# Optimization experiments

Measured on AMD Instinct MI355X. Metric: run time of the kernel, lower is better.

The kernel has to match this reference:

```python
import jax, jax.numpy as jnp
import numpy as np

N, DIM, DK, DV = 8192, 512, 128, 512


def setup_inputs() -> dict:
    key = jax.random.key(0)
    ks = jax.random.split(key, 6)
    return {
        "x": jax.random.normal(ks[0], (N, DIM), dtype=jnp.float32),
        "w_w": jax.random.normal(ks[1], (DK, DIM), dtype=jnp.float32) * (1.0 / np.sqrt(DIM)),
        "w_b": jax.random.normal(ks[2], (DK,), dtype=jnp.float32) * 0.01,
        "wv_w": jax.random.normal(ks[3], (DV, DIM), dtype=jnp.float32) * (1.0 / np.sqrt(DIM)),
        "wv_b": jax.random.normal(ks[4], (DV,), dtype=jnp.float32) * 0.01,
        "a": jax.random.normal(ks[5], (2 * DK,), dtype=jnp.float32),
    }


def reference(x, w_w, w_b, wv_w, wv_b, a):
    dk = w_b.shape[0]
    # eqx.nn.Linear: y = W @ x + b, applied per-row via vmap -> x @ W.T + b
    wx = x @ w_w.T + w_b                       # [n, dk]
    e_src = wx @ a[:dk]                        # [n], sum(wx_i * a1)
    e_dst = wx @ a[dk:]                        # [n], sum(wx_j * a2)
    logits = jax.nn.leaky_relu(e_src[:, None] + e_dst[None, :])  # [n, n]
    score = jax.nn.softmax(logits, axis=-1)    # row-wise softmax
    v = x @ wv_w.T + wv_b                      # [n, dv]
    return score @ v                           # [n, dv]
```

## Files before the change

kernel.cpp:

```cpp
#include <hip/hip_runtime.h>
#include <hip/hip_bf16.h>

#define N_   8192
#define DIM_ 512
#define DK_  128
#define DV_  512
#define L2E_ 1.44269504088896f
#define NCH_ 512
#define CHR_ 16

typedef short short8 __attribute__((ext_vector_type(8)));
typedef float f32x4  __attribute__((ext_vector_type(4)));
typedef float f32x2  __attribute__((ext_vector_type(2)));

__device__ __forceinline__ float fexp2(float x) { return __builtin_amdgcn_exp2f(x); }

__device__ __forceinline__ ushort f2bf(float f) {
    union { float f; unsigned u; } v; v.f = f;
    unsigned u = v.u;
    return (ushort)((u + 0x7FFFu + ((u >> 16) & 1u)) >> 16);
}
__device__ __forceinline__ float bf2f(ushort u) { return __uint_as_float(((unsigned)u) << 16); }
__device__ __forceinline__ float decode_max(unsigned u) {
    return __uint_as_float((u & 0x80000000u) ? (u ^ 0x80000000u) : ~u);
}

__global__ __launch_bounds__(256) void prep_kernel(const float* __restrict__ w_w,
                            const float* __restrict__ w_b, const float* __restrict__ a,
                            const float* __restrict__ wv_w,
                            float* __restrict__ u1, float* __restrict__ u2,
                            float* __restrict__ scal, ushort* __restrict__ wvbf) {
    int bid = blockIdx.x, t = threadIdx.x;
    if (bid < 2) {
        int d = bid * 256 + t;
        float s1 = 0.f, s2 = 0.f;
        for (int k = 0; k < DK_; ++k) {
            float w = w_w[k * DIM_ + d];
            s1 += w * a[k];
            s2 += w * a[DK_ + k];
        }
        u1[d] = s1; u2[d] = s2;
        if (d == 0) { float c = 0.f; for (int k = 0; k < DK_; ++k) c += w_b[k] * a[k];        scal[0] = c; }
        if (d == 1) { float c = 0.f; for (int k = 0; k < DK_; ++k) c += w_b[k] * a[DK_ + k];  scal[1] = c; }
        if (d == 2) ((unsigned*)scal)[3] = 0u;
    } else {
        int idx = (bid - 2) * 2048 + t * 8;
        f32x4 lo = *(const f32x4*)(wv_w + idx);
        f32x4 hi = *(const f32x4*)(wv_w + idx + 4);
        short8 f;
#pragma unroll
        for (int e = 0; e < 4; ++e) { f[e] = (short)f2bf(lo[e]); f[e + 4] = (short)f2bf(hi[e]); }
        *(short8*)(wvbf + idx) = f;
    }
}

__global__ __launch_bounds__(256) void e_kernel(const float* __restrict__ x,
        const float* __restrict__ u1, const float* __restrict__ u2,
        const float* __restrict__ scal, float* __restrict__ e_src, float* __restrict__ e_dst,
        ushort* __restrict__ xbf, int* __restrict__ rank, int* __restrict__ ki,
        int* __restrict__ res) {
    int wid = threadIdx.x >> 6, lane = threadIdx.x & 63;
    int row = blockIdx.x * 4 + wid;
    const float* xr = x + (size_t)row * DIM_;
    int d0 = lane * 8;
    f32x4 xa = *(const f32x4*)(xr + d0);
    f32x4 xb = *(const f32x4*)(xr + d0 + 4);
    f32x4 ua = *(const f32x4*)(u1 + d0);
    f32x4 ub = *(const f32x4*)(u1 + d0 + 4);
    f32x4 va = *(const f32x4*)(u2 + d0);
    f32x4 vb = *(const f32x4*)(u2 + d0 + 4);
    short8 xv;
#pragma unroll
    for (int e = 0; e < 4; ++e) { xv[e] = (short)f2bf(xa[e]); xv[e + 4] = (short)f2bf(xb[e]); }
    *(short8*)(xbf + (size_t)row * DIM_ + d0) = xv;
    float s1 = 0.f, s2 = 0.f;
#pragma unroll
    for (int e = 0; e < 4; ++e) {
        s1 += xa[e] * ua[e] + xb[e] * ub[e];
        s2 += xa[e] * va[e] + xb[e] * vb[e];
    }
    for (int off = 32; off; off >>= 1) { s1 += __shfl_xor(s1, off); s2 += __shfl_xor(s2, off); }
    if (lane == 0) {
        e_src[row] = s1 + scal[0];
        e_dst[row] = s2 + scal[1];
    }
    if (lane == 1) rank[row] = 0;
    if (lane == 2) ki[row] = 0;
    if (lane == 3) res[row] = 0;
}

__global__ __launch_bounds__(256) void rankv_kernel(const float* __restrict__ e_dst,
        const float* __restrict__ e_src, int* __restrict__ rank, int* __restrict__ ki,
        int* __restrict__ res, float* __restrict__ scal,
        const ushort* __restrict__ xbf, const ushort* __restrict__ wvbf,
        const float* __restrict__ wv_b, ushort* __restrict__ V) {
    int bid = blockIdx.x, t = threadIdx.x;
    if (bid < 512) {
        __shared__ float ed[512];
        __shared__ float esl[512];
        __shared__ float red[4];
        int bx = bid & 31, by = bid >> 5;
        int rbase = by * 512;
        for (int q = t; q < 512; q += 256) { ed[q] = e_dst[rbase + q]; esl[q] = e_src[rbase + q]; }
        __syncthreads();
        if (bx == 0) {
            float m = fmaxf(ed[t], ed[t + 256]);
            for (int off = 32; off; off >>= 1) m = fmaxf(m, __shfl_xor(m, off));
            if ((t & 63) == 0) red[t >> 6] = m;
            __syncthreads();
            if (t == 0) {
                m = fmaxf(fmaxf(red[0], red[1]), fmaxf(red[2], red[3]));
                unsigned u = __float_as_uint(m);
                u ^= (unsigned)(((int)u >> 31)) | 0x80000000u;
                atomicMax(((unsigned*)scal) + 3, u);
            }
        }
        int j = bx * 256 + t;
        float kj = e_dst[j];
        float kei = -e_src[j];
        float kes = e_src[j];
        int cj = 0, ci = 0, ce = 0;
#pragma unroll 8
        for (int q = 0; q < 512; ++q) {
            float v = ed[q];
            float w = esl[q];
            int r = rbase + q;
            cj += (v < kj) || (v == kj && r < j);
            ci += (v < kei);
            ce += (w < kes) || (w == kes && r < j);
        }
        atomicAdd(rank + j, cj);
        atomicAdd(ki + j, ci);
        atomicAdd(res + j, ce);
    } else {
        int vb = bid - 512;
        int wid = t >> 6, lane = t & 63;
        int ln16 = lane & 15, kg = lane >> 4;
        int jb = (vb & 31) * 256 + wid * 64;
        int cb = (vb >> 5) * 64;
        f32x4 acc[4][4] = {};
        float bias[4];
#pragma unroll
        for (int ng = 0; ng < 4; ++ng) bias[ng] = wv_b[cb + ng * 16 + ln16];
        for (int k0 = 0; k0 < DIM_; k0 += 32) {
            int kk = k0 + kg * 8;
            short8 afr[4], bfr[4];
#pragma unroll
            for (int mg = 0; mg < 4; ++mg)
                afr[mg] = *(const short8*)(xbf + (size_t)(jb + mg * 16 + ln16) * DIM_ + kk);
#pragma unroll
            for (int ng = 0; ng < 4; ++ng)
                bfr[ng] = *(const short8*)(wvbf + (size_t)(cb + ng * 16 + ln16) * DIM_ + kk);
#pragma unroll
            for (int mg = 0; mg < 4; ++mg)
#pragma unroll
                for (int ng = 0; ng < 4; ++ng)
                    acc[mg][ng] = __builtin_amdgcn_mfma_f32_16x16x32_bf16(afr[mg], bfr[ng], acc[mg][ng], 0, 0, 0);
        }
#pragma unroll
        for (int mg = 0; mg < 4; ++mg)
#pragma unroll
            for (int ng = 0; ng < 4; ++ng)
#pragma unroll
                for (int r = 0; r < 4; ++r) {
                    int j = jb + mg * 16 + kg * 4 + r;
                    int c = cb + ng * 16 + ln16;
                    V[(size_t)j * DV_ + c] = f2bf(acc[mg][ng][r] + bias[ng]);
                }
    }
}

__global__ __launch_bounds__(256) void scatter_kernel(const float* __restrict__ e_dst,
        const int* __restrict__ rank, const int* __restrict__ res, const float* __restrict__ scal,
        int* __restrict__ perm, int* __restrict__ perm_es,
        float* __restrict__ Gs1, float* __restrict__ Gs2) {
    int j = blockIdx.x * 256 + threadIdx.x;
    float M = decode_max(((const unsigned*)scal)[3]);
    int rk = rank[j];
    float d = (e_dst[j] - M) * L2E_;
    perm[rk] = j;
    perm_es[res[j]] = j;
    Gs1[rk] = fexp2(d);
    Gs2[rk] = fexp2(0.01f * d);
}

__global__ __launch_bounds__(256) void p1_kernel(const ushort* __restrict__ V,
        const int* __restrict__ perm, const float* __restrict__ Gs1, const float* __restrict__ Gs2,
        unsigned* __restrict__ Pk, float* __restrict__ C1, float* __restrict__ C2,
        float* __restrict__ C1z, float* __restrict__ C2z,
        float* __restrict__ zl2, float* __restrict__ zl1) {
    int ch = blockIdx.x >> 1, half = blockIdx.x & 1;
    int t = threadIdx.x;
    int c = half * 256 + t;
    int k0 = ch * CHR_;
    int   jj[CHR_];
    float g1[CHR_], g2[CHR_], v[CHR_];
#pragma unroll
    for (int r = 0; r < CHR_; ++r) { jj[r] = perm[k0 + r]; g1[r] = Gs1[k0 + r]; g2[r] = Gs2[k0 + r]; }
#pragma unroll
    for (int r = 0; r < CHR_; ++r) v[r] = bf2f(V[(size_t)jj[r] * DV_ + c]);
    float t1 = 0.f, t2 = 0.f;
#pragma unroll
    for (int r = 0; r < CHR_; ++r) { t1 += g1[r] * v[r]; t2 += g2[r] * v[r]; }
    float r2 = 0.f, p1r = 0.f;
#pragma unroll
    for (int r = 0; r < CHR_; ++r) {
        Pk[(size_t)(k0 + r) * DV_ + c] = (unsigned)f2bf(r2) | ((unsigned)f2bf(t1 - p1r) << 16);
        r2 += g2[r] * v[r]; p1r += g1[r] * v[r];
    }
    C1[ch * 512 + c] = t1; C2[ch * 512 + c] = t2;
    if (half == 0 && t == 0) {
        float z1t = 0.f, z2t = 0.f;
#pragma unroll
        for (int r = 0; r < CHR_; ++r) { z1t += g1[r]; z2t += g2[r]; }
        C1z[ch] = z1t; C2z[ch] = z2t;
        float zp2 = 0.f, zp1 = 0.f;
#pragma unroll
        for (int r = 0; r < CHR_; ++r) {
            zl2[k0 + r] = zp2; zl1[k0 + r] = z1t - zp1;
            zp2 += g2[r]; zp1 += g1[r];
        }
    }
    if (ch == NCH_ - 1) {
        Pk[(size_t)N_ * DV_ + c] = 0u;
        if (half == 0 && t == 0) { zl2[N_] = 0.f; zl1[N_] = 0.f; }
    }
}

__global__ __launch_bounds__(256) void p2_kernel(const float* __restrict__ C1,
        const float* __restrict__ C2, const float* __restrict__ C1z, const float* __restrict__ C2z,
        float* __restrict__ pc2, float* __restrict__ scs,
        float* __restrict__ zc2, float* __restrict__ zc1) {
    int b = blockIdx.x, t = threadIdx.x;
    if (b < 64) {
        int colL = t >> 5, s = t & 31;
        int c = b * 8 + colL;
        int base = s * 16;
        float v[16]; float seg = 0.f;
#pragma unroll
        for (int q = 0; q < 16; ++q) { v[q] = C2[(base + q) * 512 + c]; seg += v[q]; }
        float x = seg;
#pragma unroll
        for (int d = 1; d < 32; d <<= 1) { float y = __shfl_up(x, d, 32); if (s >= d) x += y; }
        float run = x - seg;
#pragma unroll
        for (int q = 0; q < 16; ++q) { pc2[(base + q) * 512 + c] = run; run += v[q]; }
        if (s == 31) pc2[NCH_ * 512 + c] = run;
    } else if (b < 128) {
        int colL = t >> 5, s = t & 31;
        int c = (b - 64) * 8 + colL;
        int base = s * 16;
        float v[16]; float seg = 0.f;
#pragma unroll
        for (int q = 0; q < 16; ++q) { v[q] = C1[(base + q) * 512 + c]; seg += v[q]; }
        float x = seg;
#pragma unroll
        for (int d = 1; d < 32; d <<= 1) { float y = __shfl_down(x, d, 32); if (s + d < 32) x += y; }
        float fwd = 0.f;
#pragma unroll
        for (int q = 0; q < 16; ++q) { fwd += v[q]; scs[(base + q) * 512 + c] = x - fwd; }
        if (s == 31) scs[NCH_ * 512 + c] = 0.f;
    } else {
        __shared__ float wt[4];
        bool pre = (b == 128);
        float v0 = pre ? C2z[t * 2] : C1z[t * 2];
        float v1 = pre ? C2z[t * 2 + 1] : C1z[t * 2 + 1];
        float seg = v0 + v1;
        int lane = t & 63, w = t >> 6;
        float x = seg;
        if (pre) {
#pragma unroll
            for (int d = 1; d < 64; d <<= 1) { float y = __shfl_up(x, d); if (lane >= d) x += y; }
            if (lane == 63) wt[w] = x;
        } else {
#pragma unroll
            for (int d = 1; d < 64; d <<= 1) { float y = __shfl_down(x, d); if (lane + d < 64) x += y; }
            if (lane == 0) wt[w] = x;
        }
        __syncthreads();
        float off = 0.f;
        if (pre) {
            for (int u = 0; u < w; ++u) off += wt[u];
            float run = off + (x - seg);
            zc2[t * 2] = run; run += v0; zc2[t * 2 + 1] = run;
            if (t == 255) zc2[NCH_] = off + x;
        } else {
            for (int u = w + 1; u < 4; ++u) off += wt[u];
            float S = off + x;
            zc1[t * 2]     = S - v0;
            zc1[t * 2 + 1] = S - v0 - v1;
            if (t == 255) zc1[NCH_] = 0.f;
        }
    }
}

__global__ __launch_bounds__(256) void out_kernel(const float* __restrict__ e_src,
        const float* __restrict__ scal, const int* __restrict__ ki,
        const int* __restrict__ perm_es,
        const float* __restrict__ zl2, const float* __restrict__ zl1,
        const float* __restrict__ zc2, const float* __restrict__ zc1,
        const float* __restrict__ pc2, const float* __restrict__ scs,
        const unsigned* __restrict__ Pk, float* __restrict__ out) {
    int t = threadIdx.x;
    float M = decode_max(((const unsigned*)scal)[3]);
    int idx0 = blockIdx.x * 16;
    int c2 = t * 2;
#pragma unroll 2
    for (int q = 0; q < 16; ++q) {
        int i = perm_es[idx0 + q];
        float es = e_src[i];
        float tt = es + M;
        float m = fmaxf(tt, 0.01f * tt);
        float F1 = fexp2((tt - m) * L2E_);
        float F2 = fexp2((0.01f * tt - m) * L2E_);
        int lo = ki[i];
        int ch = lo >> 4;
        float z = F2 * (zc2[ch] + zl2[lo]) + F1 * (zc1[ch] + zl1[lo]);
        float rz = 1.0f / z;
        const unsigned* pt = Pk + (size_t)lo * DV_;
        unsigned w0 = pt[c2], w1 = pt[c2 + 1];
        f32x2 cp = *(const f32x2*)(pc2 + ch * 512 + c2);
        f32x2 cs = *(const f32x2*)(scs + ch * 512 + c2);
        float o0 = (F2 * (cp[0] + bf2f((ushort)(w0 & 0xFFFFu))) + F1 * (cs[0] + bf2f((ushort)(w0 >> 16)))) * rz;
        float o1 = (F2 * (cp[1] + bf2f((ushort)(w1 & 0xFFFFu))) + F1 * (cs[1] + bf2f((ushort)(w1 >> 16)))) * rz;
        out[(size_t)i * DV_ + c2]     = o0;
        out[(size_t)i * DV_ + c2 + 1] = o1;
    }
}

extern "C" void kernel_launch(void* const* d_in, const int* in_sizes, int n_in,
                              void* d_out, int out_size, void* d_ws, size_t ws_size,
                              hipStream_t stream) {
    const float* x    = (const float*)d_in[0];
    const float* w_w  = (const float*)d_in[1];
    const float* w_b  = (const float*)d_in[2];
    const float* wv_w = (const float*)d_in[3];
    const float* wv_b = (const float*)d_in[4];
    const float* a    = (const float*)d_in[5];
    float* out = (float*)d_out;
    char* ws = (char*)d_ws;

    ushort*   V    = (ushort*)(ws);
    ushort*   xbf  = (ushort*)(ws + 8388608);
    unsigned* Pk   = (unsigned*)(ws + 16777216);
    char*     sm   = ws + 35651584;
    float*  u1      = (float*)(sm);
    float*  u2      = (float*)(sm + 2048);
    float*  e_src   = (float*)(sm + 4096);
    float*  e_dst   = (float*)(sm + 36864);
    float*  scal    = (float*)(sm + 69632);
    float*  Gs1     = (float*)(sm + 69888);
    float*  Gs2     = (float*)(sm + 102656);
    float*  C1      = (float*)(sm + 135424);
    float*  C2      = (float*)(sm + 1184000);
    float*  pc2     = (float*)(sm + 2232576);
    float*  scs     = (float*)(sm + 3284224);
    float*  C1z     = (float*)(sm + 4335872);
    float*  C2z     = (float*)(sm + 4337920);
    float*  zl2     = (float*)(sm + 4339968);
    float*  zl1     = (float*)(sm + 4372992);
    float*  zc2     = (float*)(sm + 4406016);
    float*  zc1     = (float*)(sm + 4410112);
    int*    perm    = (int*)  (sm + 4414208);
    int*    rank    = (int*)  (sm + 4446976);
    int*    ki      = (int*)  (sm + 4479744);
    int*    res     = (int*)  (sm + 4512512);
    int*    perm_es = (int*)  (sm + 4545280);
    ushort* wvbf    = (ushort*)(sm + 4578048);

    hipLaunchKernelGGL(prep_kernel,    dim3(130),     dim3(256), 0, stream, w_w, w_b, a, wv_w, u1, u2, scal, wvbf);
    hipLaunchKernelGGL(e_kernel,       dim3(N_ / 4),  dim3(256), 0, stream, x, u1, u2, scal, e_src, e_dst, xbf, rank, ki, res);
    hipLaunchKernelGGL(rankv_kernel,   dim3(768),     dim3(256), 0, stream, e_dst, e_src, rank, ki, res, scal, xbf, wvbf, wv_b, V);
    hipLaunchKernelGGL(scatter_kernel, dim3(32),      dim3(256), 0, stream, e_dst, rank, res, scal, perm, perm_es, Gs1, Gs2);
    hipLaunchKernelGGL(p1_kernel,      dim3(1024),    dim3(256), 0, stream, V, perm, Gs1, Gs2, Pk, C1, C2, C1z, C2z, zl2, zl1);
    hipLaunchKernelGGL(p2_kernel,      dim3(130),     dim3(256), 0, stream, C1, C2, C1z, C2z, pc2, scs, zc2, zc1);
    hipLaunchKernelGGL(out_kernel,     dim3(N_ / 16), dim3(256), 0, stream, e_src, scal, ki, perm_es, zl2, zl1, zc2, zc1, pc2, scs, Pk, out);
}
```

Measured before the change: 85.42 us.

## Recompute in-chunk partial sums in output kernel instead of materializing Pk

```diff
diff --git a/kernel.cpp b/kernel.cpp
--- a/kernel.cpp
+++ b/kernel.cpp
@@ -184,11 +184,10 @@
     Gs2[rk] = fexp2(0.01f * d);
 }
 
-__global__ __launch_bounds__(256) void p1_kernel(const ushort* __restrict__ V,
+__global__ __launch_bounds__(256) void ctot_kernel(const ushort* __restrict__ V,
         const int* __restrict__ perm, const float* __restrict__ Gs1, const float* __restrict__ Gs2,
-        unsigned* __restrict__ Pk, float* __restrict__ C1, float* __restrict__ C2,
-        float* __restrict__ C1z, float* __restrict__ C2z,
-        float* __restrict__ zl2, float* __restrict__ zl1) {
+        float* __restrict__ C1, float* __restrict__ C2,
+        float* __restrict__ C1z, float* __restrict__ C2z) {
     int ch = blockIdx.x >> 1, half = blockIdx.x & 1;
     int t = threadIdx.x;
     int c = half * 256 + t;
@@ -202,28 +201,12 @@
     float t1 = 0.f, t2 = 0.f;
 #pragma unroll
     for (int r = 0; r < CHR_; ++r) { t1 += g1[r] * v[r]; t2 += g2[r] * v[r]; }
-    float r2 = 0.f, p1r = 0.f;
-#pragma unroll
-    for (int r = 0; r < CHR_; ++r) {
-        Pk[(size_t)(k0 + r) * DV_ + c] = (unsigned)f2bf(r2) | ((unsigned)f2bf(t1 - p1r) << 16);
-        r2 += g2[r] * v[r]; p1r += g1[r] * v[r];
-    }
     C1[ch * 512 + c] = t1; C2[ch * 512 + c] = t2;
     if (half == 0 && t == 0) {
         float z1t = 0.f, z2t = 0.f;
 #pragma unroll
         for (int r = 0; r < CHR_; ++r) { z1t += g1[r]; z2t += g2[r]; }
         C1z[ch] = z1t; C2z[ch] = z2t;
-        float zp2 = 0.f, zp1 = 0.f;
-#pragma unroll
-        for (int r = 0; r < CHR_; ++r) {
-            zl2[k0 + r] = zp2; zl1[k0 + r] = z1t - zp1;
-            zp2 += g2[r]; zp1 += g1[r];
-        }
-    }
-    if (ch == NCH_ - 1) {
-        Pk[(size_t)N_ * DV_ + c] = 0u;
-        if (half == 0 && t == 0) { zl2[N_] = 0.f; zl1[N_] = 0.f; }
     }
 }
 
@@ -296,16 +279,15 @@
 
 __global__ __launch_bounds__(256) void out_kernel(const float* __restrict__ e_src,
         const float* __restrict__ scal, const int* __restrict__ ki,
-        const int* __restrict__ perm_es,
-        const float* __restrict__ zl2, const float* __restrict__ zl1,
+        const int* __restrict__ perm_es, const int* __restrict__ perm,
+        const float* __restrict__ Gs1, const float* __restrict__ Gs2,
         const float* __restrict__ zc2, const float* __restrict__ zc1,
         const float* __restrict__ pc2, const float* __restrict__ scs,
-        const unsigned* __restrict__ Pk, float* __restrict__ out) {
+        const ushort* __restrict__ V, float* __restrict__ out) {
     int t = threadIdx.x;
     float M = decode_max(((const unsigned*)scal)[3]);
     int idx0 = blockIdx.x * 16;
     int c2 = t * 2;
-#pragma unroll 2
     for (int q = 0; q < 16; ++q) {
         int i = perm_es[idx0 + q];
         float es = e_src[i];
@@ -315,16 +297,27 @@
         float F2 = fexp2((0.01f * tt - m) * L2E_);
         int lo = ki[i];
         int ch = lo >> 4;
-        float z = F2 * (zc2[ch] + zl2[lo]) + F1 * (zc1[ch] + zl1[lo]);
+        int k0 = ch << 4;
+        float a2l0 = 0.f, a2l1 = 0.f, s1l0 = 0.f, s1l1 = 0.f, z2l = 0.f, z1l = 0.f;
+        if (k0 < N_) {
+#pragma unroll 4
+            for (int r = 0; r < CHR_; ++r) {
+                int k = k0 + r;
+                int j = perm[k];
+                float g1 = Gs1[k], g2 = Gs2[k];
+                unsigned pv = *(const unsigned*)(V + (size_t)j * DV_ + c2);
+                float v0 = bf2f((ushort)(pv & 0xFFFFu));
+                float v1 = bf2f((ushort)(pv >> 16));
+                if (k < lo) { a2l0 += g2 * v0; a2l1 += g2 * v1; z2l += g2; }
+                else        { s1l0 += g1 * v0; s1l1 += g1 * v1; z1l += g1; }
+            }
+        }
+        float z = F2 * (zc2[ch] + z2l) + F1 * (zc1[ch] + z1l);
         float rz = 1.0f / z;
-        const unsigned* pt = Pk + (size_t)lo * DV_;
-        unsigned w0 = pt[c2], w1 = pt[c2 + 1];
         f32x2 cp = *(const f32x2*)(pc2 + ch * 512 + c2);
         f32x2 cs = *(const f32x2*)(scs + ch * 512 + c2);
-        float o0 = (F2 * (cp[0] + bf2f((ushort)(w0 & 0xFFFFu))) + F1 * (cs[0] + bf2f((ushort)(w0 >> 16)))) * rz;
-        float o1 = (F2 * (cp[1] + bf2f((ushort)(w1 & 0xFFFFu))) + F1 * (cs[1] + bf2f((ushort)(w1 >> 16)))) * rz;
-        out[(size_t)i * DV_ + c2]     = o0;
-        out[(size_t)i * DV_ + c2 + 1] = o1;
+        out[(size_t)i * DV_ + c2]     = (F2 * (cp[0] + a2l0) + F1 * (cs[0] + s1l0)) * rz;
+        out[(size_t)i * DV_ + c2 + 1] = (F2 * (cp[1] + a2l1) + F1 * (cs[1] + s1l1)) * rz;
     }
 }
 
@@ -340,10 +333,9 @@
     float* out = (float*)d_out;
     char* ws = (char*)d_ws;
 
-    ushort*   V    = (ushort*)(ws);
-    ushort*   xbf  = (ushort*)(ws + 8388608);
-    unsigned* Pk   = (unsigned*)(ws + 16777216);
-    char*     sm   = ws + 35651584;
+    ushort* V    = (ushort*)(ws);
+    ushort* xbf  = (ushort*)(ws + 8388608);
+    char*   sm   = ws + 16777216;
     float*  u1      = (float*)(sm);
     float*  u2      = (float*)(sm + 2048);
     float*  e_src   = (float*)(sm + 4096);
@@ -357,22 +349,20 @@
     float*  scs     = (float*)(sm + 3284224);
     float*  C1z     = (float*)(sm + 4335872);
     float*  C2z     = (float*)(sm + 4337920);
-    float*  zl2     = (float*)(sm + 4339968);
-    float*  zl1     = (float*)(sm + 4372992);
-    float*  zc2     = (float*)(sm + 4406016);
-    float*  zc1     = (float*)(sm + 4410112);
-    int*    perm    = (int*)  (sm + 4414208);
-    int*    rank    = (int*)  (sm + 4446976);
-    int*    ki      = (int*)  (sm + 4479744);
-    int*    res     = (int*)  (sm + 4512512);
-    int*    perm_es = (int*)  (sm + 4545280);
-    ushort* wvbf    = (ushort*)(sm + 4578048);
+    float*  zc2     = (float*)(sm + 4339968);
+    float*  zc1     = (float*)(sm + 4344064);
+    int*    perm    = (int*)  (sm + 4348160);
+    int*    rank    = (int*)  (sm + 4380928);
+    int*    ki      = (int*)  (sm + 4413696);
+    int*    res     = (int*)  (sm + 4446464);
+    int*    perm_es = (int*)  (sm + 4479232);
+    ushort* wvbf    = (ushort*)(sm + 4512000);
 
     hipLaunchKernelGGL(prep_kernel,    dim3(130),     dim3(256), 0, stream, w_w, w_b, a, wv_w, u1, u2, scal, wvbf);
     hipLaunchKernelGGL(e_kernel,       dim3(N_ / 4),  dim3(256), 0, stream, x, u1, u2, scal, e_src, e_dst, xbf, rank, ki, res);
     hipLaunchKernelGGL(rankv_kernel,   dim3(768),     dim3(256), 0, stream, e_dst, e_src, rank, ki, res, scal, xbf, wvbf, wv_b, V);
     hipLaunchKernelGGL(scatter_kernel, dim3(32),      dim3(256), 0, stream, e_dst, rank, res, scal, perm, perm_es, Gs1, Gs2);
-    hipLaunchKernelGGL(p1_kernel,      dim3(1024),    dim3(256), 0, stream, V, perm, Gs1, Gs2, Pk, C1, C2, C1z, C2z, zl2, zl1);
+    hipLaunchKernelGGL(ctot_kernel,    dim3(1024),    dim3(256), 0, stream, V, perm, Gs1, Gs2, C1, C2, C1z, C2z);
     hipLaunchKernelGGL(p2_kernel,      dim3(130),     dim3(256), 0, stream, C1, C2, C1z, C2z, pc2, scs, zc2, zc1);
-    hipLaunchKernelGGL(out_kernel,     dim3(N_ / 16), dim3(256), 0, stream, e_src, scal, ki, perm_es, zl2, zl1, zc2, zc1, pc2, scs, Pk, out);
-}
+    hipLaunchKernelGGL(out_kernel,     dim3(N_ / 16), dim3(256), 0, stream, e_src, scal, ki, perm_es, perm, Gs1, Gs2, zc2, zc1, pc2, scs, V, out);
+}
```

Result: slower. 133.5 us (+56.3%).
